# Kernel tuning notes

Measured on AMD Instinct MI355X. Metric: run time of the kernel, lower is better.

## Reference

```python
import jax, jax.numpy as jnp
import numpy as np

SEQ = 4096
BLOCK = 64            # sparse_block_size
BLOCKS = SEQ // BLOCK # 64 block rows/cols
NUM_ORACLES = 32
ORACLE = SEQ // NUM_ORACLES      # 128
LOCAL_BLOCKS = ORACLE // BLOCK   # 2 (sliding-window width in blocks)
PATTERN_ID = 0


def _build_block_mask(pattern_id=PATTERN_ID):
    # Mirrors DKernelPredefinedSparseAttention.__init__ create_mask((i,))
    q_pos = np.arange(BLOCKS)[:, None]
    k_pos = np.arange(BLOCKS)[None, :]
    causal = q_pos >= k_pos
    sliding = (q_pos - k_pos) < LOCAL_BLOCKS
    vert = np.zeros(BLOCKS, dtype=bool)
    real_col = int(pattern_id * ORACLE + 0.5)
    cs = real_col // BLOCK
    ce = (real_col + ORACLE) // BLOCK
    vert[cs:ce] = True
    vert[0:1] = True  # global block 0 always visible
    return causal & (sliding | vert[None, :])


def setup_inputs() -> dict:
    key = jax.random.key(0)
    kq, kk, kv = jax.random.split(key, 3)
    shape = (1, SEQ, 8, 128)  # bshd, matches module's own smoke test layout
    q = jax.random.normal(kq, shape, dtype=jnp.float32)
    k = jax.random.normal(kk, shape, dtype=jnp.float32)
    v = jax.random.normal(kv, shape, dtype=jnp.float32)
    block_mask = jnp.asarray(_build_block_mask())  # [BLOCKS, BLOCKS] bool
    return {"q": q, "k": k, "v": v, "block_mask": block_mask}


def reference(q, k, v, block_mask):
    # Expand block-level mask to token level: [S, S]
    tok_mask = jnp.repeat(jnp.repeat(block_mask, BLOCK, axis=0), BLOCK, axis=1)
    scale = 1.0 / jnp.sqrt(jnp.asarray(q.shape[-1], q.dtype))
    # bshd x bshd -> bhqk scores
    scores = jnp.einsum("bqhd,bkhd->bhqk", q, k) * scale
    neg = jnp.asarray(-1e30, scores.dtype)
    scores = jnp.where(tok_mask[None, None, :, :], scores, neg)
    probs = jax.nn.softmax(scores, axis=-1)
    out = jnp.einsum("bhqk,bkhd->bqhd", probs, v)
    return out
```

## Files before the change

kernel.cpp:

```cpp
#include <hip/hip_runtime.h>
#include <hip/hip_bf16.h>

typedef __bf16 bf16x8 __attribute__((ext_vector_type(8)));
typedef float floatx4 __attribute__((ext_vector_type(4)));

constexpr int SEQ = 4096;
constexpr int NH  = 8;
constexpr int DH  = 128;
constexpr int BLK = 64;
constexpr int QBLOCKS = SEQ / BLK;
constexpr int RS = NH * DH;
constexpr float SCALE = 0.088388347648318447f;

__device__ __forceinline__ bf16x8 load8f(const float* p) {
    float4 a = *(const float4*)p;
    float4 b = *(const float4*)(p + 4);
    bf16x8 r = { (__bf16)a.x, (__bf16)a.y, (__bf16)a.z, (__bf16)a.w,
                 (__bf16)b.x, (__bf16)b.y, (__bf16)b.z, (__bf16)b.w };
    return r;
}

__device__ __forceinline__ void stage_v(const float* __restrict__ V,
                                        int kb, int h, int n_t, int kh,
                                        __bf16* __restrict__ dst) {
    const float* base = V + (size_t)(kb * BLK + kh * 32) * RS + h * DH + n_t;
    const int nt = n_t >> 4;
    const int lbase = n_t & 15;
#pragma unroll
    for (int g = 0; g < 4; ++g) {
        bf16x8 pk;
#pragma unroll
        for (int j = 0; j < 8; ++j)
            pk[j] = (__bf16)base[(size_t)(g * 8 + j) * RS];
        __bf16* d = dst + ((size_t)((kh * 8 + nt) * 64 + lbase + 16 * g)) * 8;
        *(bf16x8*)d = pk;
    }
}

__global__ __launch_bounds__(512, 4) void sparse_attn_kernel(
    const float* __restrict__ Q,
    const float* __restrict__ K,
    const float* __restrict__ V,
    float* __restrict__ Out)
{
    const int qb    = blockIdx.x;
    const int h     = blockIdx.y;
    const int tid   = threadIdx.x;
    const int wave  = tid >> 6;
    const int lane  = tid & 63;
    const int strip = wave & 3;
    const int grp   = wave >> 2;
    const int quad  = lane >> 4;
    const int l16   = lane & 15;

    __shared__ __align__(16) __bf16 v_lds[4][2][8][64][8];
    __shared__ __align__(16) __bf16 p_lds[8][16][64];

    int blist[4];
    int nb = 0;
    {
        int cand[4] = {0, 1, qb - 1, qb};
        for (int i = 0; i < 4; ++i) {
            int b = cand[i];
            if (b < 0 || b > qb) continue;
            bool dup = false;
            for (int j = 0; j < nb; ++j) dup = dup || (blist[j] == b);
            if (!dup) blist[nb++] = b;
        }
    }

    const bool v0 = (grp < nb);
    const bool v1 = (grp + 2 < nb);
    const int kb0 = v0 ? blist[grp] : 0;
    const int kb1 = v1 ? blist[grp + 2] : 0;

    const int qrow = qb * BLK + strip * 16 + l16;
    const float* qp = Q + (size_t)qrow * RS + h * DH;
    bf16x8 qfrag[4];
#pragma unroll
    for (int s = 0; s < 4; ++s)
        qfrag[s] = load8f(qp + s * 32 + quad * 8);

    floatx4 sfrag[8];
#pragma unroll
    for (int t = 0; t < 2; ++t) {
        const bool valid = t ? v1 : v0;
        const int  kb    = t ? kb1 : kb0;
        if (valid) {
#pragma unroll
            for (int n = 0; n < 4; ++n) {
                floatx4 c = floatx4{0.f, 0.f, 0.f, 0.f};
                const float* kp =
                    K + (size_t)(kb * BLK + n * 16 + l16) * RS + h * DH;
#pragma unroll
                for (int s = 0; s < 4; ++s) {
                    bf16x8 kf = load8f(kp + s * 32 + quad * 8);
                    c = __builtin_amdgcn_mfma_f32_16x16x32_bf16(qfrag[s], kf, c, 0, 0, 0);
                }
                sfrag[t * 4 + n] = c;
            }
        } else {
#pragma unroll
            for (int n = 0; n < 4; ++n)
                sfrag[t * 4 + n] = floatx4{-1e30f, -1e30f, -1e30f, -1e30f};
        }
    }

    {
        const int t256 = tid & 255;
        const int n_t  = t256 & 127;
        const int kh   = t256 >> 7;
        const int half = tid >> 8;
        if (half < nb)
            stage_v(V, blist[half], h, n_t, kh, &v_lds[half][0][0][0][0]);
        if (half + 2 < nb)
            stage_v(V, blist[half + 2], h, n_t, kh, &v_lds[half + 2][0][0][0][0]);
    }

    float m4[4], l4[4];
#pragma unroll
    for (int r = 0; r < 4; ++r) { m4[r] = -1e30f; l4[r] = 0.f; }

    if (v0) {
#pragma unroll
        for (int r = 0; r < 4; ++r) {
            float mx = -1e30f;
#pragma unroll
            for (int i = 0; i < 8; ++i) {
                sfrag[i][r] *= SCALE;
                mx = fmaxf(mx, sfrag[i][r]);
            }
#pragma unroll
            for (int off = 1; off < 16; off <<= 1)
                mx = fmaxf(mx, __shfl_xor(mx, off, 64));
            m4[r] = mx;
        }
#pragma unroll
        for (int r = 0; r < 4; ++r) {
            float rs = 0.f;
#pragma unroll
            for (int i = 0; i < 8; ++i) {
                float p = __expf(sfrag[i][r] - m4[r]);
                sfrag[i][r] = p;
                rs += p;
            }
#pragma unroll
            for (int off = 1; off < 16; off <<= 1)
                rs += __shfl_xor(rs, off, 64);
            l4[r] = rs;
        }
    }

    floatx4 o_acc[8];
#pragma unroll
    for (int n = 0; n < 8; ++n) o_acc[n] = floatx4{0.f, 0.f, 0.f, 0.f};

    __syncthreads();

#pragma unroll
    for (int t = 0; t < 2; ++t) {
        const bool valid = t ? v1 : v0;
        if (!valid) continue;
        const int bi = grp + 2 * t;
#pragma unroll
        for (int n = 0; n < 4; ++n)
#pragma unroll
            for (int r = 0; r < 4; ++r) {
                const int prow = quad * 4 + r;
                const int col  = n * 16 + l16;
                const int idx  = (((col >> 3) ^ (prow & 7)) << 3) | (col & 7);
                p_lds[wave][prow][idx] = (__bf16)sfrag[t * 4 + n][r];
            }
#pragma unroll
        for (int s2 = 0; s2 < 2; ++s2) {
            bf16x8 pa = *(const bf16x8*)
                &p_lds[wave][l16][(((s2 * 4 + quad) ^ (l16 & 7)) << 3)];
#pragma unroll
            for (int n = 0; n < 8; ++n) {
                bf16x8 vb = *(const bf16x8*)&v_lds[bi][s2][n][lane][0];
                o_acc[n] = __builtin_amdgcn_mfma_f32_16x16x32_bf16(pa, vb, o_acc[n], 0, 0, 0);
            }
        }
    }

    __syncthreads();

    float* mrg = (float*)&v_lds[0][0][0][0][0];
    constexpr int OSTRIDE = 132;
    constexpr int OSZ     = 16 * OSTRIDE;
    constexpr int MBASE   = 4 * OSZ;
    constexpr int LBASE   = MBASE + 64;

    if (grp == 1) {
#pragma unroll
        for (int r = 0; r < 4; ++r) {
            if (l16 == 0) {
                mrg[MBASE + strip * 16 + quad * 4 + r] = m4[r];
                mrg[LBASE + strip * 16 + quad * 4 + r] = l4[r];
            }
#pragma unroll
            for (int n = 0; n < 8; ++n)
                mrg[strip * OSZ + (quad * 4 + r) * OSTRIDE + n * 16 + l16] =
                    o_acc[n][r];
        }
    }
    __syncthreads();

    if (grp == 0) {
        const int orow_base = qb * BLK + strip * 16 + quad * 4;
#pragma unroll
        for (int r = 0; r < 4; ++r) {
            const float m1 = mrg[MBASE + strip * 16 + quad * 4 + r];
            const float l1 = mrg[LBASE + strip * 16 + quad * 4 + r];
            const float M  = fmaxf(m4[r], m1);
            const float a0 = __expf(m4[r] - M);
            const float a1 = __expf(m1 - M);
            const float inv = 1.f / (a0 * l4[r] + a1 * l1);
            float* op = Out + (size_t)(orow_base + r) * RS + h * DH + l16;
#pragma unroll
            for (int n = 0; n < 8; ++n) {
                const float o1 =
                    mrg[strip * OSZ + (quad * 4 + r) * OSTRIDE + n * 16 + l16];
                op[n * 16] = (a0 * o_acc[n][r] + a1 * o1) * inv;
            }
        }
    }
}

extern "C" void kernel_launch(void* const* d_in, const int* in_sizes, int n_in,
                              void* d_out, int out_size, void* d_ws, size_t ws_size,
                              hipStream_t stream) {
    const float* Q = (const float*)d_in[0];
    const float* K = (const float*)d_in[1];
    const float* V = (const float*)d_in[2];
    float* Out = (float*)d_out;

    dim3 grid(QBLOCKS, NH);
    dim3 block(512);
    sparse_attn_kernel<<<grid, block, 0, stream>>>(Q, K, V, Out);
}
```

Before: 126.4 us.

## Pre-convert K and V to bf16 with MFMA-ready V layout in a prepass

Adds a prepass kernel that converts all of K to bf16 and transposes V into the exact LDS fragment layout, stored in global scratch arrays. The attention kernel then loads K as packed bf16 vectors and copies V into LDS with contiguous 16-byte loads, removing the strided per-element V gathers and the conversions. The cost is an extra launch and a full pass over all of K and V, even though the sparse pattern touches only a few blocks per row.

```diff
diff --git a/kernel.cpp b/kernel.cpp
--- a/kernel.cpp
+++ b/kernel.cpp
@@ -12,6 +12,9 @@
 constexpr int RS = NH * DH;
 constexpr float SCALE = 0.088388347648318447f;
 
+static __device__ __align__(16) __bf16 g_Kb[SEQ * NH * DH];
+static __device__ __align__(16) __bf16 g_Vt[SEQ * NH * DH];
+
 __device__ __forceinline__ bf16x8 load8f(const float* p) {
     float4 a = *(const float4*)p;
     float4 b = *(const float4*)(p + 4);
@@ -20,27 +23,33 @@
     return r;
 }
 
-__device__ __forceinline__ void stage_v(const float* __restrict__ V,
-                                        int kb, int h, int n_t, int kh,
-                                        __bf16* __restrict__ dst) {
-    const float* base = V + (size_t)(kb * BLK + kh * 32) * RS + h * DH + n_t;
-    const int nt = n_t >> 4;
-    const int lbase = n_t & 15;
-#pragma unroll
-    for (int g = 0; g < 4; ++g) {
-        bf16x8 pk;
-#pragma unroll
-        for (int j = 0; j < 8; ++j)
-            pk[j] = (__bf16)base[(size_t)(g * 8 + j) * RS];
-        __bf16* d = dst + ((size_t)((kh * 8 + nt) * 64 + lbase + 16 * g)) * 8;
-        *(bf16x8*)d = pk;
+constexpr int KCELLS = SEQ * NH * DH / 8;
+
+__global__ __launch_bounds__(512) void prepass_kernel(
+    const float* __restrict__ K, const float* __restrict__ V)
+{
+    const int idx = blockIdx.x * 512 + threadIdx.x;
+    if (idx < KCELLS) {
+        *(bf16x8*)&g_Kb[(size_t)idx * 8] = load8f(K + (size_t)idx * 8);
+    } else {
+        int c = idx - KCELLS;
+        const int lane = c & 63;  c >>= 6;
+        const int nt   = c & 7;   c >>= 3;
+        const int s2   = c & 1;   c >>= 1;
+        const int h    = c & 7;
+        const int kb   = c >> 3;
+        const int quad = lane >> 4, l16 = lane & 15;
+        const float* src = V + (size_t)(kb * BLK + s2 * 32 + quad * 8) * RS
+                             + h * DH + nt * 16 + l16;
+        bf16x8 r;
+#pragma unroll
+        for (int j = 0; j < 8; ++j) r[j] = (__bf16)src[(size_t)j * RS];
+        *(bf16x8*)&g_Vt[(size_t)(idx - KCELLS) * 8] = r;
     }
 }
 
 __global__ __launch_bounds__(512, 4) void sparse_attn_kernel(
     const float* __restrict__ Q,
-    const float* __restrict__ K,
-    const float* __restrict__ V,
     float* __restrict__ Out)
 {
     const int qb    = blockIdx.x;
@@ -90,11 +99,11 @@
 #pragma unroll
             for (int n = 0; n < 4; ++n) {
                 floatx4 c = floatx4{0.f, 0.f, 0.f, 0.f};
-                const float* kp =
-                    K + (size_t)(kb * BLK + n * 16 + l16) * RS + h * DH;
+                const __bf16* kp =
+                    g_Kb + (size_t)(kb * BLK + n * 16 + l16) * RS + h * DH;
 #pragma unroll
                 for (int s = 0; s < 4; ++s) {
-                    bf16x8 kf = load8f(kp + s * 32 + quad * 8);
+                    bf16x8 kf = *(const bf16x8*)(kp + s * 32 + quad * 8);
                     c = __builtin_amdgcn_mfma_f32_16x16x32_bf16(qfrag[s], kf, c, 0, 0, 0);
                 }
                 sfrag[t * 4 + n] = c;
@@ -107,14 +116,18 @@
     }
 
     {
-        const int t256 = tid & 255;
-        const int n_t  = t256 & 127;
-        const int kh   = t256 >> 7;
-        const int half = tid >> 8;
-        if (half < nb)
-            stage_v(V, blist[half], h, n_t, kh, &v_lds[half][0][0][0][0]);
-        if (half + 2 < nb)
-            stage_v(V, blist[half + 2], h, n_t, kh, &v_lds[half + 2][0][0][0][0]);
+        __bf16* ldsf = &v_lds[0][0][0][0][0];
+#pragma unroll
+        for (int i = 0; i < 8; ++i) {
+            const int ti = i >> 1;
+            if (ti < nb) {
+                const int c = i * 512 + tid;
+                const bf16x8 d = *(const bf16x8*)(g_Vt
+                    + (size_t)(blist[ti] * NH + h) * 8192
+                    + (size_t)((i & 1) * 512 + tid) * 8);
+                *(bf16x8*)(ldsf + (size_t)c * 8) = d;
+            }
+        }
     }
 
     float m4[4], l4[4];
@@ -235,7 +248,9 @@
     const float* V = (const float*)d_in[2];
     float* Out = (float*)d_out;
 
+    dim3 pgrid(2 * KCELLS / 512);
+    prepass_kernel<<<pgrid, dim3(512), 0, stream>>>(K, V);
+
     dim3 grid(QBLOCKS, NH);
-    dim3 block(512);
-    sparse_attn_kernel<<<grid, block, 0, stream>>>(Q, K, V, Out);
-}
+    sparse_attn_kernel<<<grid, dim3(512), 0, stream>>>(Q, Out);
+}
```

After: 122.5 us. 1.03x faster.
